# Kernel optimization log

Hardware: AMD Instinct MI355X
Metric: run time of the kernel (lower is better)

## Reference

```python
import jax, jax.numpy as jnp
import numpy as np

H = 512   # hidden_dim
B = 1024  # batch
D = 256   # history length


def setup_inputs() -> dict:
    key = jax.random.key(0)
    k1, k2, k3, k4, k5, k6 = jax.random.split(key, 6)
    return {
        "h_tilde": jax.random.normal(k1, (B, H), dtype=jnp.float32),
        "c_t": jax.random.normal(k2, (B, H), dtype=jnp.float32),
        "h_history": jax.random.normal(k3, (B, D, H), dtype=jnp.float32),
        # learned parameters (nn.Linear stores weight as [out, in]; y = x @ W.T)
        "Waq": jax.random.normal(k4, (H, 2 * H), dtype=jnp.float32) * (1.0 / np.sqrt(2 * H)),
        "Wah": jax.random.normal(k5, (H, H), dtype=jnp.float32) * (1.0 / np.sqrt(H)),
        "ba": jnp.zeros((H,), dtype=jnp.float32),
        "v_t": jax.random.normal(k6, (H,), dtype=jnp.float32),
    }


def reference(h_tilde, c_t, h_history, Waq, Wah, ba, v_t):
    # q_t = [h_tilde ; c_t] -> [B, 2H]; project to [B, H]
    q_t = jnp.concatenate([h_tilde, c_t], axis=1)
    q_proj = q_t @ Waq.T                         # [B, H]
    h_proj = jnp.einsum('bdh,gh->bdg', h_history, Wah)  # [B, D, H]
    # broadcast add + tanh: the large [B, D, H] intermediate
    score_pre = jnp.tanh(q_proj[:, None, :] + h_proj + ba)
    alpha_unscaled = jnp.einsum('bdh,h->bd', score_pre, v_t)  # [B, D]
    alpha = jax.nn.softmax(alpha_unscaled, axis=1)            # [B, D]
    e_t = jnp.einsum('bd,bdh->bh', alpha, h_history)          # [B, H]
    return (e_t, alpha)
```

## Files before the change

### kernel.cpp

```cpp
#include <hip/hip_runtime.h>
#include <hip/hip_bf16.h>

#define HDIM 512
#define BDIM 1024
#define DDIM 256
#define MTOT (BDIM * DDIM)

typedef _Float16 half8 __attribute__((ext_vector_type(8)));
typedef float f32x4 __attribute__((ext_vector_type(4)));

__device__ __forceinline__ float ftanh(float x) {
    float e = __expf(2.0f * x);
    float d = e + 1.0f;
    float r;
    asm("v_rcp_f32 %0, %1" : "=v"(r) : "v"(d));
    return 1.0f - 2.0f * r;
}

__device__ __forceinline__ void gl_lds16(const _Float16* src, _Float16* dst) {
    __builtin_amdgcn_global_load_lds((const __attribute__((address_space(1))) void*)src,
                                     (__attribute__((address_space(3))) void*)dst,
                                     16, 0, 0);
}

__global__ __launch_bounds__(256) void k_prep(const float* __restrict__ h_tilde,
                                              const float* __restrict__ c_t,
                                              const float* __restrict__ Waq,
                                              const float* __restrict__ ba,
                                              const float* __restrict__ Wah,
                                              float* __restrict__ qb,
                                              _Float16* __restrict__ W16) {
    __shared__ float qs[16][1024];
    int t = threadIdx.x;
    if (blockIdx.x >= 256) {
        int n = (blockIdx.x - 256) * 256 + t;
        int p = n >> 9, r = n & 511;
        int kb = r >> 6, kp = (r >> 4) & 3, g = r & 15;
        int c = p >> 1, kh = p & 1;
        const float* src = Wah + (size_t)(c * 16 + g) * 512 + kh * 256 + kb * 32 + kp * 8;
        float4 v0 = *(const float4*)src;
        float4 v1 = *(const float4*)(src + 4);
        half8 h;
        h[0] = (_Float16)v0.x; h[1] = (_Float16)v0.y; h[2] = (_Float16)v0.z; h[3] = (_Float16)v0.w;
        h[4] = (_Float16)v1.x; h[5] = (_Float16)v1.y; h[6] = (_Float16)v1.z; h[7] = (_Float16)v1.w;
        *(half8*)&W16[(size_t)n * 8] = h;
        return;
    }
    int bt = blockIdx.x >> 2, gq = blockIdx.x & 3;
    int b0 = bt * 16;
    #pragma unroll
    for (int i = 0; i < 16; i++) {
        int idx = t + i * 256;
        int row = idx >> 8, k = (idx & 255) * 4;
        float4 v;
        if (k < 512) v = *(const float4*)&h_tilde[(b0 + row) * 512 + k];
        else         v = *(const float4*)&c_t[(b0 + row) * 512 + k - 512];
        *(float4*)&qs[row][k] = v;
    }
    __syncthreads();
    int g = gq * 128 + (t & 127);
    int bh = t >> 7;
    float acc[8] = {0.f, 0.f, 0.f, 0.f, 0.f, 0.f, 0.f, 0.f};
    const float4* wp = (const float4*)&Waq[(size_t)g * 1024];
    #pragma unroll 2
    for (int k4 = 0; k4 < 256; k4++) {
        float4 wv = wp[k4];
        #pragma unroll
        for (int j = 0; j < 8; j++) {
            float4 q = *(const float4*)&qs[bh * 8 + j][k4 * 4];
            acc[j] += q.x * wv.x + q.y * wv.y + q.z * wv.z + q.w * wv.w;
        }
    }
    float bav = ba[g];
    #pragma unroll
    for (int j = 0; j < 8; j++)
        qb[(b0 + bh * 8 + j) * 512 + g] = acc[j] + bav;
}

__global__ __launch_bounds__(256, 4) void k_logits(const float* __restrict__ hist,
                                                   const float* __restrict__ qb,
                                                   const _Float16* __restrict__ W16,
                                                   const float* __restrict__ v_t,
                                                   float* __restrict__ logits,
                                                   float* __restrict__ eparts,
                                                   float* __restrict__ ms) {
    __shared__ _Float16 Wb[4][4096];
    __shared__ float qbs[512];
    __shared__ float vsh[512];
    __shared__ float lsh[64];

    int t = threadIdx.x;
    int w = t >> 6, lane = t & 63, l15 = lane & 15, l4 = lane >> 4;
    int bx = blockIdx.x;
    size_t m_base = (size_t)bx * 64;
    int b = bx >> 2;
    int offp = ((bx >> 3) & 3) * 16;

    qbs[t] = qb[b * 512 + t];
    qbs[t + 256] = qb[b * 512 + 256 + t];
    vsh[t] = v_t[t];
    vsh[t + 256] = v_t[256 + t];

    #pragma unroll
    for (int pp = 0; pp < 2; pp++) {
        const _Float16* wc = W16 + (size_t)((pp + offp) & 63) * 4096;
        #pragma unroll
        for (int sg = 0; sg < 2; sg++)
            gl_lds16(wc + ((size_t)(w * 2 + sg) * 64 + lane) * 8,
                     &Wb[pp][(w * 2 + sg) * 512]);
    }

    half8 afr[16];
    const float* xb = hist + (m_base + w * 16 + l15) * 512 + l4 * 8;
    {
        float4 xr0[4], xr1[4];
        #pragma unroll
        for (int u = 0; u < 4; u++) {
            xr0[u] = *(const float4*)(xb + u * 32);
            xr1[u] = *(const float4*)(xb + u * 32 + 4);
        }
        #pragma unroll
        for (int kb = 0; kb < 16; kb++) {
            const int slot = kb & 3;
            float4 v0 = xr0[slot];
            float4 v1 = xr1[slot];
            if (kb + 4 < 16) {
                xr0[slot] = *(const float4*)(xb + (kb + 4) * 32);
                xr1[slot] = *(const float4*)(xb + (kb + 4) * 32 + 4);
            }
            half8 h;
            h[0] = (_Float16)v0.x; h[1] = (_Float16)v0.y; h[2] = (_Float16)v0.z; h[3] = (_Float16)v0.w;
            h[4] = (_Float16)v1.x; h[5] = (_Float16)v1.y; h[6] = (_Float16)v1.z; h[7] = (_Float16)v1.w;
            afr[kb] = h;
        }
    }

    float S[4] = {0.f, 0.f, 0.f, 0.f};
    f32x4 tac = (f32x4){0.f, 0.f, 0.f, 0.f};

    asm volatile("s_waitcnt lgkmcnt(0)" ::: "memory");

#define PHASE_BODY(P, VMS, ISSUE, KH)                                          \
    {                                                                          \
        const int p_ = (P);                                                    \
        asm volatile("s_waitcnt vmcnt(" VMS ")" ::: "memory");                 \
        __builtin_amdgcn_s_barrier();                                          \
        if (ISSUE) {                                                           \
            const _Float16* wc_ = W16 + (size_t)((p_ + 2 + offp) & 63) * 4096; \
            _Float16* wd_ = Wb[(p_ + 2) & 3];                                  \
            _Pragma("unroll")                                                  \
            for (int sg_ = 0; sg_ < 2; sg_++)                                  \
                gl_lds16(wc_ + ((size_t)(w * 2 + sg_) * 64 + lane) * 8,        \
                         &wd_[(w * 2 + sg_) * 512]);                           \
        }                                                                      \
        const int cc_ = ((p_ + offp) & 63) >> 1;                               \
        const _Float16* bufp_ = &Wb[p_ & 3][lane * 8];                         \
        if ((KH) == 0) tac = (f32x4){0.f, 0.f, 0.f, 0.f};                      \
        __builtin_amdgcn_s_setprio(1);                                         \
        _Pragma("unroll")                                                      \
        for (int kb_ = 0; kb_ < 8; kb_++) {                                    \
            half8 bf = *(const half8*)(bufp_ + kb_ * 512);                     \
            tac = __builtin_amdgcn_mfma_f32_16x16x32_f16(afr[(KH) * 8 + kb_], bf, tac, 0, 0, 0); \
        }                                                                      \
        __builtin_amdgcn_s_setprio(0);                                         \
        if ((KH) == 1) {                                                       \
            float qv = qbs[cc_ * 16 + l15];                                    \
            float vv = vsh[cc_ * 16 + l15];                                    \
            _Pragma("unroll")                                                  \
            for (int j_ = 0; j_ < 4; j_++)                                     \
                S[j_] += ftanh(tac[j_] + qv) * vv;                             \
        }                                                                      \
    }

    for (int q = 0; q < 31; q++) {
        PHASE_BODY(2 * q,     "2", true, 0)
        PHASE_BODY(2 * q + 1, "2", true, 1)
    }
    PHASE_BODY(62, "2", false, 0)
    PHASE_BODY(63, "0", false, 1)
#undef PHASE_BODY

    #pragma unroll
    for (int j = 0; j < 4; j++) {
        float s = S[j];
        s += __shfl_xor(s, 1, 64);
        s += __shfl_xor(s, 2, 64);
        s += __shfl_xor(s, 4, 64);
        s += __shfl_xor(s, 8, 64);
        if (l15 == 0) {
            logits[m_base + w * 16 + l4 * 4 + j] = s;
            lsh[w * 16 + l4 * 4 + j] = s;
        }
    }
    __syncthreads();

    float lv = lsh[lane];
    float mb = lv;
    mb = fmaxf(mb, __shfl_xor(mb, 1, 64));
    mb = fmaxf(mb, __shfl_xor(mb, 2, 64));
    mb = fmaxf(mb, __shfl_xor(mb, 4, 64));
    mb = fmaxf(mb, __shfl_xor(mb, 8, 64));
    mb = fmaxf(mb, __shfl_xor(mb, 16, 64));
    mb = fmaxf(mb, __shfl_xor(mb, 32, 64));
    float eb = __expf(lv - mb);
    float sb = eb;
    sb += __shfl_xor(sb, 1, 64);
    sb += __shfl_xor(sb, 2, 64);
    sb += __shfl_xor(sb, 4, 64);
    sb += __shfl_xor(sb, 8, 64);
    sb += __shfl_xor(sb, 16, 64);
    sb += __shfl_xor(sb, 32, 64);

    float coef = __expf(lsh[w * 16 + l15] - mb);
    float* ews = (float*)Wb;
    #pragma unroll
    for (int kb = 0; kb < 16; kb++) {
        float ep[8];
        half8 x = afr[kb];
        #pragma unroll
        for (int e2 = 0; e2 < 8; e2++) ep[e2] = coef * (float)x[e2];
        #pragma unroll
        for (int e2 = 0; e2 < 8; e2++) {
            ep[e2] += __shfl_xor(ep[e2], 1, 64);
            ep[e2] += __shfl_xor(ep[e2], 2, 64);
            ep[e2] += __shfl_xor(ep[e2], 4, 64);
            ep[e2] += __shfl_xor(ep[e2], 8, 64);
        }
        if (l15 == 0) {
            #pragma unroll
            for (int e2 = 0; e2 < 8; e2++)
                ews[w * 512 + kb * 32 + l4 * 8 + e2] = ep[e2];
        }
    }
    __syncthreads();
    float v0 = ews[t] + ews[512 + t] + ews[1024 + t] + ews[1536 + t];
    float v1 = ews[256 + t] + ews[768 + t] + ews[1280 + t] + ews[1792 + t];
    eparts[(size_t)bx * 512 + t] = v0;
    eparts[(size_t)bx * 512 + 256 + t] = v1;
    if (t == 0) { ms[bx * 2] = mb; ms[bx * 2 + 1] = sb; }
}

__global__ __launch_bounds__(256) void k_comb(const float* __restrict__ logits,
                                              const float* __restrict__ eparts,
                                              const float* __restrict__ ms,
                                              float* __restrict__ out) {
    int b = blockIdx.x, t = threadIdx.x;
    float m0 = ms[(4 * b + 0) * 2], s0 = ms[(4 * b + 0) * 2 + 1];
    float m1 = ms[(4 * b + 1) * 2], s1 = ms[(4 * b + 1) * 2 + 1];
    float m2 = ms[(4 * b + 2) * 2], s2 = ms[(4 * b + 2) * 2 + 1];
    float m3 = ms[(4 * b + 3) * 2], s3 = ms[(4 * b + 3) * 2 + 1];
    float m = fmaxf(fmaxf(m0, m1), fmaxf(m2, m3));
    float w0 = __expf(m0 - m), w1 = __expf(m1 - m);
    float w2 = __expf(m2 - m), w3 = __expf(m3 - m);
    float Sb = w0 * s0 + w1 * s1 + w2 * s2 + w3 * s3;
    float l = logits[b * 256 + t];
    out[BDIM * HDIM + b * 256 + t] = __expf(l - m) / Sb;
    const float* ep = eparts + (size_t)(4 * b) * 512;
    float a0 = w0 * ep[t] + w1 * ep[512 + t] + w2 * ep[1024 + t] + w3 * ep[1536 + t];
    float a1 = w0 * ep[256 + t] + w1 * ep[768 + t] + w2 * ep[1280 + t] + w3 * ep[1792 + t];
    out[b * 512 + t] = a0 / Sb;
    out[b * 512 + 256 + t] = a1 / Sb;
}

extern "C" void kernel_launch(void* const* d_in, const int* in_sizes, int n_in,
                              void* d_out, int out_size, void* d_ws, size_t ws_size,
                              hipStream_t stream) {
    const float* h_tilde = (const float*)d_in[0];
    const float* c_t     = (const float*)d_in[1];
    const float* hist    = (const float*)d_in[2];
    const float* Waq     = (const float*)d_in[3];
    const float* Wah     = (const float*)d_in[4];
    const float* ba      = (const float*)d_in[5];
    const float* v_t     = (const float*)d_in[6];
    float* out = (float*)d_out;

    char* ws = (char*)d_ws;
    float*    qb     = (float*)ws;
    _Float16* W16    = (_Float16*)(ws + (2u << 20));
    float*    logits = (float*)(ws + (3u << 20));
    float*    eparts = (float*)(ws + (4u << 20));
    float*    ms     = (float*)(ws + (12u << 20));

    k_prep<<<384, 256, 0, stream>>>(h_tilde, c_t, Waq, ba, Wah, qb, W16);
    k_logits<<<4096, 256, 0, stream>>>(hist, qb, W16, v_t, logits, eparts, ms);
    k_comb<<<1024, 256, 0, stream>>>(logits, eparts, ms, out);
}
```

Before: 350.1 us.

## Switch logits GEMM to 32x32x16 MFMA with 128-row tiles per block

The logits kernel now uses 32x32x16 f16 MFMA and each block handles 128 history rows instead of 64, so every wave owns 32 rows with the full 512-wide K held in registers. The Wah repacking changes to match the new B-fragment layout, and the block softmax partials and combine step are reduced from four parts per batch row to two. The aim is more reuse of each LDS-staged weight tile, fewer blocks and less partial-combine work. The cost is roughly double the register footprint (32 half8 fragments plus 16 accumulators), with launch bounds lowered to 2 blocks per SM, which reduces occupancy.

```diff
diff --git a/kernel.cpp b/kernel.cpp
--- a/kernel.cpp
+++ b/kernel.cpp
@@ -7,7 +7,7 @@
 #define MTOT (BDIM * DDIM)
 
 typedef _Float16 half8 __attribute__((ext_vector_type(8)));
-typedef float f32x4 __attribute__((ext_vector_type(4)));
+typedef float f32x16 __attribute__((ext_vector_type(16)));
 
 __device__ __forceinline__ float ftanh(float x) {
     float e = __expf(2.0f * x);
@@ -34,10 +34,11 @@
     int t = threadIdx.x;
     if (blockIdx.x >= 256) {
         int n = (blockIdx.x - 256) * 256 + t;
-        int p = n >> 9, r = n & 511;
-        int kb = r >> 6, kp = (r >> 4) & 3, g = r & 15;
-        int c = p >> 1, kh = p & 1;
-        const float* src = Wah + (size_t)(c * 16 + g) * 512 + kh * 256 + kb * 32 + kp * 8;
+        int p = n >> 9, g = n & 511;
+        int i = g >> 6, l = g & 63;
+        int col = (p >> 2) * 32 + (l & 31);
+        int k = (p & 3) * 128 + i * 16 + (l >> 5) * 8;
+        const float* src = Wah + (size_t)col * 512 + k;
         float4 v0 = *(const float4*)src;
         float4 v1 = *(const float4*)(src + 4);
         half8 h;
@@ -77,7 +78,7 @@
         qb[(b0 + bh * 8 + j) * 512 + g] = acc[j] + bav;
 }
 
-__global__ __launch_bounds__(256, 4) void k_logits(const float* __restrict__ hist,
+__global__ __launch_bounds__(256, 2) void k_logits(const float* __restrict__ hist,
                                                    const float* __restrict__ qb,
                                                    const _Float16* __restrict__ W16,
                                                    const float* __restrict__ v_t,
@@ -87,14 +88,16 @@
     __shared__ _Float16 Wb[4][4096];
     __shared__ float qbs[512];
     __shared__ float vsh[512];
-    __shared__ float lsh[64];
+    __shared__ float lsh[128];
+    __shared__ float wredM[2];
+    __shared__ float wredS[2];
 
     int t = threadIdx.x;
-    int w = t >> 6, lane = t & 63, l15 = lane & 15, l4 = lane >> 4;
+    int w = t >> 6, lane = t & 63, l31 = lane & 31, lh = lane >> 5;
     int bx = blockIdx.x;
-    size_t m_base = (size_t)bx * 64;
-    int b = bx >> 2;
-    int offp = ((bx >> 3) & 3) * 16;
+    size_t m_base = (size_t)bx * 128;
+    int b = bx >> 1;
+    int offp = ((bx >> 1) & 7) * 8;
 
     qbs[t] = qb[b * 512 + t];
     qbs[t + 256] = qb[b * 512 + 256 + t];
@@ -110,23 +113,23 @@
                      &Wb[pp][(w * 2 + sg) * 512]);
     }
 
-    half8 afr[16];
-    const float* xb = hist + (m_base + w * 16 + l15) * 512 + l4 * 8;
+    half8 afr[32];
+    const float* xb = hist + (m_base + w * 32 + l31) * 512 + lh * 8;
     {
         float4 xr0[4], xr1[4];
         #pragma unroll
         for (int u = 0; u < 4; u++) {
-            xr0[u] = *(const float4*)(xb + u * 32);
-            xr1[u] = *(const float4*)(xb + u * 32 + 4);
-        }
-        #pragma unroll
-        for (int kb = 0; kb < 16; kb++) {
+            xr0[u] = *(const float4*)(xb + u * 16);
+            xr1[u] = *(const float4*)(xb + u * 16 + 4);
+        }
+        #pragma unroll
+        for (int kb = 0; kb < 32; kb++) {
             const int slot = kb & 3;
             float4 v0 = xr0[slot];
             float4 v1 = xr1[slot];
-            if (kb + 4 < 16) {
-                xr0[slot] = *(const float4*)(xb + (kb + 4) * 32);
-                xr1[slot] = *(const float4*)(xb + (kb + 4) * 32 + 4);
+            if (kb + 4 < 32) {
+                xr0[slot] = *(const float4*)(xb + (kb + 4) * 16);
+                xr1[slot] = *(const float4*)(xb + (kb + 4) * 16 + 4);
             }
             half8 h;
             h[0] = (_Float16)v0.x; h[1] = (_Float16)v0.y; h[2] = (_Float16)v0.z; h[3] = (_Float16)v0.w;
@@ -135,12 +138,14 @@
         }
     }
 
-    float S[4] = {0.f, 0.f, 0.f, 0.f};
-    f32x4 tac = (f32x4){0.f, 0.f, 0.f, 0.f};
+    float S[16];
+    #pragma unroll
+    for (int r = 0; r < 16; r++) S[r] = 0.f;
+    f32x16 tac;
 
     asm volatile("s_waitcnt lgkmcnt(0)" ::: "memory");
 
-#define PHASE_BODY(P, VMS, ISSUE, KH)                                          \
+#define PHASE_BODY(P, VMS, ISSUE, KQ)                                          \
     {                                                                          \
         const int p_ = (P);                                                    \
         asm volatile("s_waitcnt vmcnt(" VMS ")" ::: "memory");                 \
@@ -153,48 +158,57 @@
                 gl_lds16(wc_ + ((size_t)(w * 2 + sg_) * 64 + lane) * 8,        \
                          &wd_[(w * 2 + sg_) * 512]);                           \
         }                                                                      \
-        const int cc_ = ((p_ + offp) & 63) >> 1;                               \
+        const int cc_ = ((p_ + offp) & 63) >> 2;                               \
         const _Float16* bufp_ = &Wb[p_ & 3][lane * 8];                         \
-        if ((KH) == 0) tac = (f32x4){0.f, 0.f, 0.f, 0.f};                      \
+        if ((KQ) == 0) {                                                       \
+            _Pragma("unroll")                                                  \
+            for (int r_ = 0; r_ < 16; r_++) tac[r_] = 0.f;                     \
+        }                                                                      \
         __builtin_amdgcn_s_setprio(1);                                         \
         _Pragma("unroll")                                                      \
-        for (int kb_ = 0; kb_ < 8; kb_++) {                                    \
-            half8 bf = *(const half8*)(bufp_ + kb_ * 512);                     \
-            tac = __builtin_amdgcn_mfma_f32_16x16x32_f16(afr[(KH) * 8 + kb_], bf, tac, 0, 0, 0); \
+        for (int i_ = 0; i_ < 8; i_++) {                                       \
+            half8 bf = *(const half8*)(bufp_ + i_ * 512);                      \
+            tac = __builtin_amdgcn_mfma_f32_32x32x16_f16(afr[(KQ) * 8 + i_], bf, tac, 0, 0, 0); \
         }                                                                      \
         __builtin_amdgcn_s_setprio(0);                                         \
-        if ((KH) == 1) {                                                       \
-            float qv = qbs[cc_ * 16 + l15];                                    \
-            float vv = vsh[cc_ * 16 + l15];                                    \
+        if ((KQ) == 3) {                                                       \
+            float qv = qbs[cc_ * 32 + l31];                                    \
+            float vv = vsh[cc_ * 32 + l31];                                    \
             _Pragma("unroll")                                                  \
-            for (int j_ = 0; j_ < 4; j_++)                                     \
-                S[j_] += ftanh(tac[j_] + qv) * vv;                             \
+            for (int r_ = 0; r_ < 16; r_++)                                    \
+                S[r_] += ftanh(tac[r_] + qv) * vv;                             \
         }                                                                      \
     }
 
-    for (int q = 0; q < 31; q++) {
-        PHASE_BODY(2 * q,     "2", true, 0)
-        PHASE_BODY(2 * q + 1, "2", true, 1)
-    }
-    PHASE_BODY(62, "2", false, 0)
-    PHASE_BODY(63, "0", false, 1)
+    for (int q = 0; q < 15; q++) {
+        PHASE_BODY(4 * q,     "2", true, 0)
+        PHASE_BODY(4 * q + 1, "2", true, 1)
+        PHASE_BODY(4 * q + 2, "2", true, 2)
+        PHASE_BODY(4 * q + 3, "2", true, 3)
+    }
+    PHASE_BODY(60, "2", true,  0)
+    PHASE_BODY(61, "2", true,  1)
+    PHASE_BODY(62, "2", false, 2)
+    PHASE_BODY(63, "0", false, 3)
 #undef PHASE_BODY
 
     #pragma unroll
-    for (int j = 0; j < 4; j++) {
-        float s = S[j];
+    for (int r = 0; r < 16; r++) {
+        float s = S[r];
         s += __shfl_xor(s, 1, 64);
         s += __shfl_xor(s, 2, 64);
         s += __shfl_xor(s, 4, 64);
         s += __shfl_xor(s, 8, 64);
-        if (l15 == 0) {
-            logits[m_base + w * 16 + l4 * 4 + j] = s;
-            lsh[w * 16 + l4 * 4 + j] = s;
-        }
-    }
-    __syncthreads();
-
-    float lv = lsh[lane];
+        s += __shfl_xor(s, 16, 64);
+        if (l31 == 0) {
+            int row = w * 32 + (r & 3) + 8 * (r >> 2) + 4 * lh;
+            logits[m_base + row] = s;
+            lsh[row] = s;
+        }
+    }
+    __syncthreads();
+
+    float lv = lsh[t & 127];
     float mb = lv;
     mb = fmaxf(mb, __shfl_xor(mb, 1, 64));
     mb = fmaxf(mb, __shfl_xor(mb, 2, 64));
@@ -202,19 +216,25 @@
     mb = fmaxf(mb, __shfl_xor(mb, 8, 64));
     mb = fmaxf(mb, __shfl_xor(mb, 16, 64));
     mb = fmaxf(mb, __shfl_xor(mb, 32, 64));
-    float eb = __expf(lv - mb);
-    float sb = eb;
+    if (lane == 0 && w < 2) wredM[w] = mb;
+    __syncthreads();
+    mb = fmaxf(wredM[0], wredM[1]);
+    float e = __expf(lv - mb);
+    float sb = e;
     sb += __shfl_xor(sb, 1, 64);
     sb += __shfl_xor(sb, 2, 64);
     sb += __shfl_xor(sb, 4, 64);
     sb += __shfl_xor(sb, 8, 64);
     sb += __shfl_xor(sb, 16, 64);
     sb += __shfl_xor(sb, 32, 64);
-
-    float coef = __expf(lsh[w * 16 + l15] - mb);
+    if (lane == 0 && w < 2) wredS[w] = sb;
+    __syncthreads();
+    sb = wredS[0] + wredS[1];
+
+    float coef = __expf(lsh[w * 32 + l31] - mb);
     float* ews = (float*)Wb;
     #pragma unroll
-    for (int kb = 0; kb < 16; kb++) {
+    for (int kb = 0; kb < 32; kb++) {
         float ep[8];
         half8 x = afr[kb];
         #pragma unroll
@@ -225,11 +245,12 @@
             ep[e2] += __shfl_xor(ep[e2], 2, 64);
             ep[e2] += __shfl_xor(ep[e2], 4, 64);
             ep[e2] += __shfl_xor(ep[e2], 8, 64);
-        }
-        if (l15 == 0) {
+            ep[e2] += __shfl_xor(ep[e2], 16, 64);
+        }
+        if (l31 == 0) {
             #pragma unroll
             for (int e2 = 0; e2 < 8; e2++)
-                ews[w * 512 + kb * 32 + l4 * 8 + e2] = ep[e2];
+                ews[w * 512 + kb * 16 + lh * 8 + e2] = ep[e2];
         }
     }
     __syncthreads();
@@ -245,19 +266,16 @@
                                               const float* __restrict__ ms,
                                               float* __restrict__ out) {
     int b = blockIdx.x, t = threadIdx.x;
-    float m0 = ms[(4 * b + 0) * 2], s0 = ms[(4 * b + 0) * 2 + 1];
-    float m1 = ms[(4 * b + 1) * 2], s1 = ms[(4 * b + 1) * 2 + 1];
-    float m2 = ms[(4 * b + 2) * 2], s2 = ms[(4 * b + 2) * 2 + 1];
-    float m3 = ms[(4 * b + 3) * 2], s3 = ms[(4 * b + 3) * 2 + 1];
-    float m = fmaxf(fmaxf(m0, m1), fmaxf(m2, m3));
+    float m0 = ms[4 * b], s0 = ms[4 * b + 1];
+    float m1 = ms[4 * b + 2], s1 = ms[4 * b + 3];
+    float m = fmaxf(m0, m1);
     float w0 = __expf(m0 - m), w1 = __expf(m1 - m);
-    float w2 = __expf(m2 - m), w3 = __expf(m3 - m);
-    float Sb = w0 * s0 + w1 * s1 + w2 * s2 + w3 * s3;
+    float Sb = w0 * s0 + w1 * s1;
     float l = logits[b * 256 + t];
     out[BDIM * HDIM + b * 256 + t] = __expf(l - m) / Sb;
-    const float* ep = eparts + (size_t)(4 * b) * 512;
-    float a0 = w0 * ep[t] + w1 * ep[512 + t] + w2 * ep[1024 + t] + w3 * ep[1536 + t];
-    float a1 = w0 * ep[256 + t] + w1 * ep[768 + t] + w2 * ep[1280 + t] + w3 * ep[1792 + t];
+    const float* ep = eparts + (size_t)(2 * b) * 512;
+    float a0 = w0 * ep[t] + w1 * ep[512 + t];
+    float a1 = w0 * ep[256 + t] + w1 * ep[768 + t];
     out[b * 512 + t] = a0 / Sb;
     out[b * 512 + 256 + t] = a1 / Sb;
 }
@@ -279,9 +297,9 @@
     _Float16* W16    = (_Float16*)(ws + (2u << 20));
     float*    logits = (float*)(ws + (3u << 20));
     float*    eparts = (float*)(ws + (4u << 20));
-    float*    ms     = (float*)(ws + (12u << 20));
+    float*    ms     = (float*)(ws + (8u << 20));
 
     k_prep<<<384, 256, 0, stream>>>(h_tilde, c_t, Waq, ba, Wah, qb, W16);
-    k_logits<<<4096, 256, 0, stream>>>(hist, qb, W16, v_t, logits, eparts, ms);
+    k_logits<<<2048, 256, 0, stream>>>(hist, qb, W16, v_t, logits, eparts, ms);
     k_comb<<<1024, 256, 0, stream>>>(logits, eparts, ms, out);
 }
```

New measurement: 357.6 us. +2.1%, slower.
